# Performance work log

Measured on AMD Instinct MI355X. Metric: run time of the kernel, lower is better.

Reference implementation:

```python
import jax, jax.numpy as jnp
import numpy as np

B, HH, WW, C = 1, 96, 96, 128
HEADS, K = 4, 7

def setup_inputs() -> dict:
    key = jax.random.key(0)
    ks = jax.random.split(key, 6)
    def lin(k, o, i):
        return jax.random.normal(k, (o, i), jnp.float32) * (1.0 / np.sqrt(i))
    return {
        "x": jax.random.normal(ks[0], (B, HH, WW, C), jnp.float32),
        "qkv_w": lin(ks[1], 3 * C, C),
        "qkv_b": jnp.zeros((3 * C,), jnp.float32),
        "proj_w": lin(ks[2], C, C),
        "proj_b": jnp.zeros((C,), jnp.float32),
        "fc1_w": lin(ks[3], 4 * C, C),
        "fc1_b": jnp.zeros((4 * C,), jnp.float32),
        "fc2_w": lin(ks[4], C, 4 * C),
        "fc2_b": jnp.zeros((C,), jnp.float32),
    }

def _na2d(q, k, v):
    # q,k,v: [B, heads, H, W, hd]; NATTEN 2D neighborhood attention,
    # kernel K, stride 1, dilation 1, non-causal. Windows are clamped at
    # borders so each query attends to exactly K*K in-bounds keys.
    Bq, h, Hs, Ws, hd = q.shape
    start_h = jnp.clip(jnp.arange(Hs) - K // 2, 0, Hs - K)
    idx_h = start_h[:, None] + jnp.arange(K)  # [H, K]
    start_w = jnp.clip(jnp.arange(Ws) - K // 2, 0, Ws - K)
    idx_w = start_w[:, None] + jnp.arange(K)  # [W, K]
    I = idx_h[:, None, :, None]  # -> [H, W, K, K] broadcast
    J = idx_w[None, :, None, :]
    k_nb = k[:, :, I, J, :]  # [B, heads, H, W, K, K, hd]
    v_nb = v[:, :, I, J, :]
    scale = jnp.asarray(hd, q.dtype) ** -0.5
    logits = jnp.einsum('bhijd,bhijkld->bhijkl', q, k_nb) * scale
    attn = jax.nn.softmax(logits.reshape(Bq, h, Hs, Ws, K * K), axis=-1)
    attn = attn.reshape(Bq, h, Hs, Ws, K, K)
    return jnp.einsum('bhijkl,bhijkld->bhijd', attn, v_nb)

def reference(x, qkv_w, qkv_b, proj_w, proj_b, fc1_w, fc1_b, fc2_w, fc2_b):
    Bq, Hs, Ws, Cc = x.shape
    hd = Cc // HEADS
    qkv = x @ qkv_w.T + qkv_b  # [B,H,W,3C]
    q, k, v = jnp.split(qkv, 3, axis=-1)
    def to_heads(t):
        return t.reshape(Bq, Hs, Ws, HEADS, hd).transpose(0, 3, 1, 2, 4)
    o = _na2d(to_heads(q), to_heads(k), to_heads(v))  # [B,heads,H,W,hd]
    o = o.transpose(0, 2, 3, 1, 4).reshape(Bq, Hs, Ws, Cc)
    x0 = o @ proj_w.T + proj_b
    h1 = jax.nn.gelu(x0 @ fc1_w.T + fc1_b, approximate=False)
    return h1 @ fc2_w.T + fc2_b
```

## Files before the change

kernel.cpp:

```cpp
#include <hip/hip_runtime.h>

typedef __bf16 bf16_t;
typedef __bf16 bf16x8 __attribute__((ext_vector_type(8)));
typedef __bf16 bf16x4 __attribute__((ext_vector_type(4)));
typedef float f32x4 __attribute__((ext_vector_type(4)));

#define HH 96
#define WW 96
#define CC 128
#define HEADS 4
#define HD 32
#define TOK (HH * WW)
#define PLANE (TOK * CC)
#define KW 7
#define KK 49

#define W_QKV 0
#define W_PROJ 49152
#define W_FC1 65536
#define W_FC2 131072
#define W_TOT 196608

__device__ __forceinline__ bf16x8 cvt8(const float* __restrict__ p) {
    const f32x4 a = *(const f32x4*)p;
    const f32x4 b = *(const f32x4*)(p + 4);
    bf16x8 r;
    r[0] = (bf16_t)a[0]; r[1] = (bf16_t)a[1]; r[2] = (bf16_t)a[2]; r[3] = (bf16_t)a[3];
    r[4] = (bf16_t)b[0]; r[5] = (bf16_t)b[1]; r[6] = (bf16_t)b[2]; r[7] = (bf16_t)b[3];
    return r;
}

template <int NT>
__device__ __forceinline__ void mmaN(const bf16_t* __restrict__ A, int lda,
                                     const bf16_t* __restrict__ W, int ldb,
                                     int K, f32x4* acc) {
    const int lane = threadIdx.x & 63;
    const bf16_t* ap = A + (lane & 15) * lda + ((lane >> 4) * 8);
    const bf16_t* bp = W + (lane & 15) * ldb + ((lane >> 4) * 8);
    for (int k0 = 0; k0 < K; k0 += 32) {
        bf16x8 a = *(const bf16x8*)(ap + k0);
#pragma unroll
        for (int t = 0; t < NT; t++) {
            bf16x8 b = *(const bf16x8*)(bp + t * 16 * ldb + k0);
            acc[t] = __builtin_amdgcn_mfma_f32_16x16x32_bf16(a, b, acc[t], 0, 0, 0);
        }
    }
}

__global__ __launch_bounds__(256) void k_cvt(const float* __restrict__ qkv_w,
                                             const float* __restrict__ proj_w,
                                             const float* __restrict__ fc1_w,
                                             const float* __restrict__ fc2_w,
                                             bf16_t* __restrict__ wb) {
    const int base = (blockIdx.x * 256 + threadIdx.x) * 4;
    const float* src;
    if (base < W_PROJ)      src = qkv_w + base;
    else if (base < W_FC1)  src = proj_w + (base - W_PROJ);
    else if (base < W_FC2)  src = fc1_w + (base - W_FC1);
    else                    src = fc2_w + (base - W_FC2);
    const f32x4 a = *(const f32x4*)src;
    bf16x4 r;
    r[0] = (bf16_t)a[0]; r[1] = (bf16_t)a[1]; r[2] = (bf16_t)a[2]; r[3] = (bf16_t)a[3];
    *(bf16x4*)(wb + base) = r;
}

__global__ __launch_bounds__(256) void k_qkv(const float* __restrict__ x,
                                             const bf16_t* __restrict__ wb,
                                             const float* __restrict__ bias,
                                             bf16_t* __restrict__ q,
                                             bf16_t* __restrict__ k,
                                             bf16_t* __restrict__ v) {
    const int wid = blockIdx.x * 4 + (threadIdx.x >> 6);
    const int m0 = (wid / 6) * 16;
    const int n0 = (wid % 6) * 64;
    const int lane = threadIdx.x & 63;
    const float* ap = x + (m0 + (lane & 15)) * CC + ((lane >> 4) * 8);
    const bf16_t* bp = wb + (n0 + (lane & 15)) * CC + ((lane >> 4) * 8);
    f32x4 acc[4] = {};
    for (int k0 = 0; k0 < CC; k0 += 32) {
        bf16x8 a = cvt8(ap + k0);
#pragma unroll
        for (int t = 0; t < 4; t++) {
            bf16x8 b = *(const bf16x8*)(bp + t * 16 * CC + k0);
            acc[t] = __builtin_amdgcn_mfma_f32_16x16x32_bf16(a, b, acc[t], 0, 0, 0);
        }
    }
#pragma unroll
    for (int t = 0; t < 4; t++) {
        const int n = n0 + t * 16 + (lane & 15);
        const float bb = bias[n];
        const int part = n >> 7;
        const int c = n & 127;
        bf16_t* dst = (part == 0) ? q : (part == 1) ? k : v;
#pragma unroll
        for (int r = 0; r < 4; r++) {
            const int m = m0 + (lane >> 4) * 4 + r;
            dst[m * CC + c] = (bf16_t)(acc[t][r] + bb);
        }
    }
}

#define PATCH 10
#define PSZ 100
#define NPAD 112
#define STR 136
__global__ __launch_bounds__(256) void k_na2d(bf16_t* __restrict__ qo,
                                              const bf16_t* __restrict__ kg,
                                              const bf16_t* __restrict__ vg) {
    __shared__ __align__(16) bf16_t regA[(NPAD + 16) * STR];
    __shared__ __align__(16) bf16_t Pbuf[4 * 16 * STR];
    bf16_t* ks  = regA;
    bf16_t* qs  = regA + NPAD * STR;
    bf16_t* vst = regA;

    const int tid = threadIdx.x;
    const int w = tid >> 6, lane = tid & 63;
    const int g = lane >> 4, li = lane & 15;
    const int bi = blockIdx.x / 24, bj = blockIdx.x % 24;
    const int i0 = bi * 4, j0 = bj * 4;
    const int pr0 = min(max(i0 - 3, 0), HH - PATCH);
    const int pc0 = min(max(j0 - 3, 0), WW - PATCH);

    for (int idx = tid; idx < PSZ * 16; idx += 256) {
        const int row = idx >> 4, c8 = idx & 15;
        const int pi = row / PATCH, pj = row - PATCH * pi;
        *(bf16x8*)(ks + row * STR + c8 * 8) =
            *(const bf16x8*)(kg + ((pr0 + pi) * WW + (pc0 + pj)) * CC + c8 * 8);
    }
    {
        const int row = tid >> 4, c8 = tid & 15;
        const int ti = row >> 2, tj = row & 3;
        *(bf16x8*)(qs + row * STR + c8 * 8) =
            *(const bf16x8*)(qo + ((i0 + ti) * WW + (j0 + tj)) * CC + c8 * 8);
    }
    __syncthreads();

    const int head = w;
    f32x4 lg[7];
    {
        const bf16x8 aq = *(const bf16x8*)(qs + li * STR + head * HD + g * 8);
#pragma unroll
        for (int t = 0; t < 7; t++) {
            const bf16x8 bk = *(const bf16x8*)(ks + (t * 16 + li) * STR + head * HD + g * 8);
            lg[t] = __builtin_amdgcn_mfma_f32_16x16x32_bf16(aq, bk, (f32x4){0.f,0.f,0.f,0.f}, 0, 0, 0);
        }
    }

    int lr[4], lc[4];
#pragma unroll
    for (int r = 0; r < 4; r++) {
        const int m = g * 4 + r;
        const int i = i0 + (m >> 2), j = j0 + (m & 3);
        lr[r] = min(max(i - 3, 0), HH - KW) - pr0;
        lc[r] = min(max(j - 3, 0), WW - KW) - pc0;
    }
    const float scale = 0.17677669529663687f;
#pragma unroll
    for (int t = 0; t < 7; t++) {
        const int col = t * 16 + li;
        const int pi = col / PATCH, pj = col - PATCH * pi;
#pragma unroll
        for (int r = 0; r < 4; r++) {
            const bool valid = (col < PSZ) &&
                               ((unsigned)(pi - lr[r]) <= 6u) &&
                               ((unsigned)(pj - lc[r]) <= 6u);
            lg[t][r] = valid ? lg[t][r] * scale : -1e30f;
        }
    }
    f32x4 mx = lg[0], sm;
#pragma unroll
    for (int t = 1; t < 7; t++)
#pragma unroll
        for (int r = 0; r < 4; r++) mx[r] = fmaxf(mx[r], lg[t][r]);
#pragma unroll
    for (int off = 8; off; off >>= 1)
#pragma unroll
        for (int r = 0; r < 4; r++) mx[r] = fmaxf(mx[r], __shfl_xor(mx[r], off));
#pragma unroll
    for (int r = 0; r < 4; r++) sm[r] = 0.f;
#pragma unroll
    for (int t = 0; t < 7; t++)
#pragma unroll
        for (int r = 0; r < 4; r++) {
            lg[t][r] = __expf(lg[t][r] - mx[r]);
            sm[r] += lg[t][r];
        }
#pragma unroll
    for (int off = 8; off; off >>= 1)
#pragma unroll
        for (int r = 0; r < 4; r++) sm[r] += __shfl_xor(sm[r], off);
#pragma unroll
    for (int r = 0; r < 4; r++) sm[r] = 1.f / sm[r];

    bf16_t* Pw = Pbuf + w * 16 * STR;
#pragma unroll
    for (int t = 0; t < 7; t++)
#pragma unroll
        for (int r = 0; r < 4; r++)
            Pw[(g * 4 + r) * STR + t * 16 + li] = (bf16_t)(lg[t][r] * sm[r]);
    *(bf16x4*)(Pw + (lane >> 2) * STR + NPAD + (lane & 3) * 4) = (bf16x4){0,0,0,0};

    __syncthreads();
    for (int idx = tid; idx < PSZ * 16; idx += 256) {
        const int c8 = idx / PSZ;
        const int p  = idx - c8 * PSZ;
        const int pi = p / PATCH, pj = p - PATCH * pi;
        const bf16x8 t = *(const bf16x8*)(vg + ((pr0 + pi) * WW + (pc0 + pj)) * CC + c8 * 8);
#pragma unroll
        for (int e = 0; e < 8; e++) vst[(c8 * 8 + e) * STR + p] = t[e];
    }
    for (int idx = tid; idx < 128 * 8; idx += 256) {
        const int row = idx >> 3, c4 = idx & 7;
        *(bf16x4*)(vst + row * STR + PSZ + c4 * 4) = (bf16x4){0,0,0,0};
    }
    __syncthreads();

    f32x4 oA[2] = {};
#pragma unroll
    for (int ks0 = 0; ks0 < 128; ks0 += 32) {
        const bf16x8 a = *(const bf16x8*)(Pw + li * STR + ks0 + g * 8);
#pragma unroll
        for (int t2 = 0; t2 < 2; t2++) {
            const bf16x8 b = *(const bf16x8*)(vst + (head * HD + t2 * 16 + li) * STR + ks0 + g * 8);
            oA[t2] = __builtin_amdgcn_mfma_f32_16x16x32_bf16(a, b, oA[t2], 0, 0, 0);
        }
    }
#pragma unroll
    for (int t2 = 0; t2 < 2; t2++)
#pragma unroll
        for (int r = 0; r < 4; r++) {
            const int m = g * 4 + r;
            const int i = i0 + (m >> 2), j = j0 + (m & 3);
            qo[(i * WW + j) * CC + head * HD + t2 * 16 + li] = (bf16_t)oA[t2][r];
        }
}

__global__ __launch_bounds__(256) void k_proj(const bf16_t* __restrict__ o,
                                              const bf16_t* __restrict__ wb,
                                              const float* __restrict__ bias,
                                              bf16_t* __restrict__ x0) {
    const int wid = blockIdx.x * 4 + (threadIdx.x >> 6);
    const int m0 = (wid / 2) * 16;
    const int n0 = (wid % 2) * 64;
    f32x4 acc[4] = {};
    mmaN<4>(o + m0 * CC, CC, wb + n0 * CC, CC, CC, acc);
    const int lane = threadIdx.x & 63;
#pragma unroll
    for (int t = 0; t < 4; t++) {
        const int n = n0 + t * 16 + (lane & 15);
        const float bb = bias[n];
#pragma unroll
        for (int r = 0; r < 4; r++) {
            const int m = m0 + (lane >> 4) * 4 + r;
            x0[m * CC + n] = (bf16_t)(acc[t][r] + bb);
        }
    }
}

#define H1S 520
__global__ __launch_bounds__(256) void k_mlp(const bf16_t* __restrict__ x0,
                                             const bf16_t* __restrict__ w1,
                                             const float* __restrict__ b1,
                                             const bf16_t* __restrict__ w2,
                                             const float* __restrict__ b2,
                                             float* __restrict__ out) {
    __shared__ __align__(16) bf16_t h1s[16 * H1S];
    const int wv = threadIdx.x >> 6;
    const int lane = threadIdx.x & 63;
    const int m0 = blockIdx.x * 16;

    {
        f32x4 acc[8] = {};
        mmaN<8>(x0 + m0 * CC, CC, w1 + (wv * 128) * CC, CC, CC, acc);
#pragma unroll
        for (int t = 0; t < 8; t++) {
            const int n = wv * 128 + t * 16 + (lane & 15);
            const float bb = b1[n];
#pragma unroll
            for (int r = 0; r < 4; r++) {
                const int m = (lane >> 4) * 4 + r;
                const float xv = acc[t][r] + bb;
                const float u = 0.7978845608028654f * (xv + 0.044715f * xv * xv * xv);
                const float e = __expf(2.f * u);
                const float gg = 0.5f * xv * (2.f - 2.f / (e + 1.f));
                h1s[m * H1S + n] = (bf16_t)gg;
            }
        }
    }
    __syncthreads();

    {
        f32x4 acc[2] = {};
        mmaN<2>(h1s, H1S, w2 + (wv * 32) * (4 * CC), 4 * CC, 4 * CC, acc);
#pragma unroll
        for (int t = 0; t < 2; t++) {
            const int n = wv * 32 + t * 16 + (lane & 15);
            const float bb = b2[n];
#pragma unroll
            for (int r = 0; r < 4; r++) {
                const int m = (lane >> 4) * 4 + r;
                float xv = acc[t][r] + bb;
                xv = fminf(fmaxf(xv, -1e4f), 1e4f);
                out[(m0 + m) * CC + n] = xv;
            }
        }
    }
}

extern "C" void kernel_launch(void* const* d_in, const int* in_sizes, int n_in,
                              void* d_out, int out_size, void* d_ws, size_t ws_size,
                              hipStream_t stream) {
    const float* x      = (const float*)d_in[0];
    const float* qkv_w  = (const float*)d_in[1];
    const float* qkv_b  = (const float*)d_in[2];
    const float* proj_w = (const float*)d_in[3];
    const float* proj_b = (const float*)d_in[4];
    const float* fc1_w  = (const float*)d_in[5];
    const float* fc1_b  = (const float*)d_in[6];
    const float* fc2_w  = (const float*)d_in[7];
    const float* fc2_b  = (const float*)d_in[8];

    bf16_t* qo = (bf16_t*)d_out;
    bf16_t* ws = (bf16_t*)d_ws;
    bf16_t* kb = ws;
    bf16_t* vb = ws + PLANE;
    bf16_t* wb = ws + 2 * PLANE;
    bf16_t* x0 = kb;

    k_cvt <<<192,  256, 0, stream>>>(qkv_w, proj_w, fc1_w, fc2_w, wb);
    k_qkv <<<864,  256, 0, stream>>>(x, wb + W_QKV, qkv_b, qo, kb, vb);
    k_na2d<<<576,  256, 0, stream>>>(qo, kb, vb);
    k_proj<<<288,  256, 0, stream>>>(qo, wb + W_PROJ, proj_b, x0);
    k_mlp <<<576,  256, 0, stream>>>(x0, wb + W_FC1, fc1_b, wb + W_FC2, fc2_b,
                                     (float*)d_out);
}
```

Baseline: 130.9 us.

## Fuse neighborhood attention, projection and MLP into one kernel; fold weight conversion into QKV

Collapses five launches into two. The weight-conversion kernel is merged into the QKV GEMM, which now converts qkv_w from fp32 on the fly and writes Q as fp32 into the output buffer. The attention kernel then runs the output projection, fc1+GELU and fc2 on its 16-token tile in shared memory, so the o and x0 intermediates never go through global memory. In exchange each attention block does more serial work with more syncs, and QKV blocks re-convert fp32 qkv weights per block.

```diff
diff --git a/kernel.cpp b/kernel.cpp
--- a/kernel.cpp
+++ b/kernel.cpp
@@ -13,13 +13,21 @@
 #define TOK (HH * WW)
 #define PLANE (TOK * CC)
 #define KW 7
-#define KK 49
-
-#define W_QKV 0
-#define W_PROJ 49152
-#define W_FC1 65536
-#define W_FC2 131072
-#define W_TOT 196608
+
+#define W_PROJ 0
+#define W_FC1  16384
+#define W_FC2  81920
+#define W_TOT  147456
+
+#define PATCH 10
+#define PSZ 100
+#define NPAD 112
+#define STR 136
+#define H1S 520
+
+#define REGA_ELE ((NPAD + 16) * STR)
+#define PBUF_ELE (4 * 16 * STR)
+#define SMEM_BYTES ((REGA_ELE + PBUF_ELE) * 2)
 
 __device__ __forceinline__ bf16x8 cvt8(const float* __restrict__ p) {
     const f32x4 a = *(const f32x4*)p;
@@ -47,79 +55,88 @@
     }
 }
 
-__global__ __launch_bounds__(256) void k_cvt(const float* __restrict__ qkv_w,
+__global__ __launch_bounds__(256) void k_qkv(const float* __restrict__ x,
+                                             const float* __restrict__ qkv_w,
+                                             const float* __restrict__ qkv_b,
                                              const float* __restrict__ proj_w,
                                              const float* __restrict__ fc1_w,
                                              const float* __restrict__ fc2_w,
+                                             float* __restrict__ qf,
+                                             bf16_t* __restrict__ kb,
+                                             bf16_t* __restrict__ vb,
                                              bf16_t* __restrict__ wb) {
-    const int base = (blockIdx.x * 256 + threadIdx.x) * 4;
-    const float* src;
-    if (base < W_PROJ)      src = qkv_w + base;
-    else if (base < W_FC1)  src = proj_w + (base - W_PROJ);
-    else if (base < W_FC2)  src = fc1_w + (base - W_FC1);
-    else                    src = fc2_w + (base - W_FC2);
-    const f32x4 a = *(const f32x4*)src;
-    bf16x4 r;
-    r[0] = (bf16_t)a[0]; r[1] = (bf16_t)a[1]; r[2] = (bf16_t)a[2]; r[3] = (bf16_t)a[3];
-    *(bf16x4*)(wb + base) = r;
-}
-
-__global__ __launch_bounds__(256) void k_qkv(const float* __restrict__ x,
-                                             const bf16_t* __restrict__ wb,
-                                             const float* __restrict__ bias,
-                                             bf16_t* __restrict__ q,
-                                             bf16_t* __restrict__ k,
-                                             bf16_t* __restrict__ v) {
-    const int wid = blockIdx.x * 4 + (threadIdx.x >> 6);
-    const int m0 = (wid / 6) * 16;
-    const int n0 = (wid % 6) * 64;
-    const int lane = threadIdx.x & 63;
-    const float* ap = x + (m0 + (lane & 15)) * CC + ((lane >> 4) * 8);
-    const bf16_t* bp = wb + (n0 + (lane & 15)) * CC + ((lane >> 4) * 8);
-    f32x4 acc[4] = {};
+    const int tid = threadIdx.x, bid = blockIdx.x;
+    {
+        const int idx = bid * 256 + tid;
+        if (idx < W_TOT / 4) {
+            const int base = idx * 4;
+            const float* src;
+            if (base < W_FC1)      src = proj_w + base;
+            else if (base < W_FC2) src = fc1_w + (base - W_FC1);
+            else                   src = fc2_w + (base - W_FC2);
+            const f32x4 a = *(const f32x4*)src;
+            bf16x4 r;
+            r[0] = (bf16_t)a[0]; r[1] = (bf16_t)a[1];
+            r[2] = (bf16_t)a[2]; r[3] = (bf16_t)a[3];
+            *(bf16x4*)(wb + base) = r;
+        }
+    }
+    const int w = tid >> 6, lane = tid & 63;
+    const int g = lane >> 4, li = lane & 15;
+    const int m0 = bid * 16;
+    const float* ap = x + (m0 + li) * CC + g * 8;
+    const float* bp = qkv_w + (w * 96 + li) * CC + g * 8;
+    f32x4 acc[6] = {};
     for (int k0 = 0; k0 < CC; k0 += 32) {
         bf16x8 a = cvt8(ap + k0);
 #pragma unroll
-        for (int t = 0; t < 4; t++) {
-            bf16x8 b = *(const bf16x8*)(bp + t * 16 * CC + k0);
+        for (int t = 0; t < 6; t++) {
+            bf16x8 b = cvt8(bp + t * 16 * CC + k0);
             acc[t] = __builtin_amdgcn_mfma_f32_16x16x32_bf16(a, b, acc[t], 0, 0, 0);
         }
     }
 #pragma unroll
-    for (int t = 0; t < 4; t++) {
-        const int n = n0 + t * 16 + (lane & 15);
-        const float bb = bias[n];
-        const int part = n >> 7;
-        const int c = n & 127;
-        bf16_t* dst = (part == 0) ? q : (part == 1) ? k : v;
+    for (int t = 0; t < 6; t++) {
+        const int n = w * 96 + t * 16 + li;
+        const float bb = qkv_b[n];
+        const int part = n >> 7, c = n & 127;
 #pragma unroll
         for (int r = 0; r < 4; r++) {
-            const int m = m0 + (lane >> 4) * 4 + r;
-            dst[m * CC + c] = (bf16_t)(acc[t][r] + bb);
-        }
-    }
-}
-
-#define PATCH 10
-#define PSZ 100
-#define NPAD 112
-#define STR 136
-__global__ __launch_bounds__(256) void k_na2d(bf16_t* __restrict__ qo,
-                                              const bf16_t* __restrict__ kg,
-                                              const bf16_t* __restrict__ vg) {
-    __shared__ __align__(16) bf16_t regA[(NPAD + 16) * STR];
-    __shared__ __align__(16) bf16_t Pbuf[4 * 16 * STR];
-    bf16_t* ks  = regA;
-    bf16_t* qs  = regA + NPAD * STR;
-    bf16_t* vst = regA;
+            const int m = m0 + g * 4 + r;
+            const float val = acc[t][r] + bb;
+            if (part == 0)      qf[m * CC + c] = val;
+            else if (part == 1) kb[m * CC + c] = (bf16_t)val;
+            else                vb[m * CC + c] = (bf16_t)val;
+        }
+    }
+}
+
+__global__ __launch_bounds__(256, 3) void k_attn_mlp(
+        float* __restrict__ qof,
+        const bf16_t* __restrict__ kg,
+        const bf16_t* __restrict__ vg,
+        const bf16_t* __restrict__ wb,
+        const float* __restrict__ proj_b,
+        const float* __restrict__ fc1_b,
+        const float* __restrict__ fc2_b) {
+    __shared__ __align__(16) bf16_t smem[REGA_ELE + PBUF_ELE];
+    bf16_t* ks   = smem;
+    bf16_t* qs   = smem + NPAD * STR;
+    bf16_t* vst  = smem;
+    bf16_t* h1s  = smem;
+    bf16_t* Pbuf = smem + REGA_ELE;
+    bf16_t* o_s  = Pbuf;
+    bf16_t* x0s  = Pbuf + 16 * STR;
 
     const int tid = threadIdx.x;
     const int w = tid >> 6, lane = tid & 63;
     const int g = lane >> 4, li = lane & 15;
-    const int bi = blockIdx.x / 24, bj = blockIdx.x % 24;
+    const int bid = blockIdx.x;
+    const int bi = bid / 24, bj = bid % 24;
     const int i0 = bi * 4, j0 = bj * 4;
     const int pr0 = min(max(i0 - 3, 0), HH - PATCH);
     const int pc0 = min(max(j0 - 3, 0), WW - PATCH);
+    const int head = w;
 
     for (int idx = tid; idx < PSZ * 16; idx += 256) {
         const int row = idx >> 4, c8 = idx & 15;
@@ -131,11 +148,10 @@
         const int row = tid >> 4, c8 = tid & 15;
         const int ti = row >> 2, tj = row & 3;
         *(bf16x8*)(qs + row * STR + c8 * 8) =
-            *(const bf16x8*)(qo + ((i0 + ti) * WW + (j0 + tj)) * CC + c8 * 8);
-    }
-    __syncthreads();
-
-    const int head = w;
+            cvt8(qof + ((i0 + ti) * WW + (j0 + tj)) * CC + c8 * 8);
+    }
+    __syncthreads();
+
     f32x4 lg[7];
     {
         const bf16x8 aq = *(const bf16x8*)(qs + li * STR + head * HD + g * 8);
@@ -145,7 +161,6 @@
             lg[t] = __builtin_amdgcn_mfma_f32_16x16x32_bf16(aq, bk, (f32x4){0.f,0.f,0.f,0.f}, 0, 0, 0);
         }
     }
-
     int lr[4], lc[4];
 #pragma unroll
     for (int r = 0; r < 4; r++) {
@@ -199,11 +214,10 @@
         for (int r = 0; r < 4; r++)
             Pw[(g * 4 + r) * STR + t * 16 + li] = (bf16_t)(lg[t][r] * sm[r]);
     *(bf16x4*)(Pw + (lane >> 2) * STR + NPAD + (lane & 3) * 4) = (bf16x4){0,0,0,0};
-
-    __syncthreads();
+    __syncthreads();
+
     for (int idx = tid; idx < PSZ * 16; idx += 256) {
-        const int c8 = idx / PSZ;
-        const int p  = idx - c8 * PSZ;
+        const int c8 = idx / PSZ, p = idx - c8 * PSZ;
         const int pi = p / PATCH, pj = p - PATCH * pi;
         const bf16x8 t = *(const bf16x8*)(vg + ((pr0 + pi) * WW + (pc0 + pj)) * CC + c8 * 8);
 #pragma unroll
@@ -225,60 +239,39 @@
             oA[t2] = __builtin_amdgcn_mfma_f32_16x16x32_bf16(a, b, oA[t2], 0, 0, 0);
         }
     }
+    __syncthreads();
+
 #pragma unroll
     for (int t2 = 0; t2 < 2; t2++)
 #pragma unroll
-        for (int r = 0; r < 4; r++) {
-            const int m = g * 4 + r;
-            const int i = i0 + (m >> 2), j = j0 + (m & 3);
-            qo[(i * WW + j) * CC + head * HD + t2 * 16 + li] = (bf16_t)oA[t2][r];
-        }
-}
-
-__global__ __launch_bounds__(256) void k_proj(const bf16_t* __restrict__ o,
-                                              const bf16_t* __restrict__ wb,
-                                              const float* __restrict__ bias,
-                                              bf16_t* __restrict__ x0) {
-    const int wid = blockIdx.x * 4 + (threadIdx.x >> 6);
-    const int m0 = (wid / 2) * 16;
-    const int n0 = (wid % 2) * 64;
-    f32x4 acc[4] = {};
-    mmaN<4>(o + m0 * CC, CC, wb + n0 * CC, CC, CC, acc);
-    const int lane = threadIdx.x & 63;
-#pragma unroll
-    for (int t = 0; t < 4; t++) {
-        const int n = n0 + t * 16 + (lane & 15);
-        const float bb = bias[n];
-#pragma unroll
-        for (int r = 0; r < 4; r++) {
-            const int m = m0 + (lane >> 4) * 4 + r;
-            x0[m * CC + n] = (bf16_t)(acc[t][r] + bb);
-        }
-    }
-}
-
-#define H1S 520
-__global__ __launch_bounds__(256) void k_mlp(const bf16_t* __restrict__ x0,
-                                             const bf16_t* __restrict__ w1,
-                                             const float* __restrict__ b1,
-                                             const bf16_t* __restrict__ w2,
-                                             const float* __restrict__ b2,
-                                             float* __restrict__ out) {
-    __shared__ __align__(16) bf16_t h1s[16 * H1S];
-    const int wv = threadIdx.x >> 6;
-    const int lane = threadIdx.x & 63;
-    const int m0 = blockIdx.x * 16;
+        for (int r = 0; r < 4; r++)
+            o_s[(g * 4 + r) * STR + head * HD + t2 * 16 + li] = (bf16_t)oA[t2][r];
+    __syncthreads();
+
+    {
+        f32x4 acc[2] = {};
+        mmaN<2>(o_s, STR, wb + W_PROJ + (w * 32) * CC, CC, CC, acc);
+#pragma unroll
+        for (int t = 0; t < 2; t++) {
+            const int n = w * 32 + t * 16 + li;
+            const float bb = proj_b[n];
+#pragma unroll
+            for (int r = 0; r < 4; r++)
+                x0s[(g * 4 + r) * STR + n] = (bf16_t)(acc[t][r] + bb);
+        }
+    }
+    __syncthreads();
 
     {
         f32x4 acc[8] = {};
-        mmaN<8>(x0 + m0 * CC, CC, w1 + (wv * 128) * CC, CC, CC, acc);
+        mmaN<8>(x0s, STR, wb + W_FC1 + (w * 128) * CC, CC, CC, acc);
 #pragma unroll
         for (int t = 0; t < 8; t++) {
-            const int n = wv * 128 + t * 16 + (lane & 15);
-            const float bb = b1[n];
+            const int n = w * 128 + t * 16 + li;
+            const float bb = fc1_b[n];
 #pragma unroll
             for (int r = 0; r < 4; r++) {
-                const int m = (lane >> 4) * 4 + r;
+                const int m = g * 4 + r;
                 const float xv = acc[t][r] + bb;
                 const float u = 0.7978845608028654f * (xv + 0.044715f * xv * xv * xv);
                 const float e = __expf(2.f * u);
@@ -291,17 +284,18 @@
 
     {
         f32x4 acc[2] = {};
-        mmaN<2>(h1s, H1S, w2 + (wv * 32) * (4 * CC), 4 * CC, 4 * CC, acc);
+        mmaN<2>(h1s, H1S, wb + W_FC2 + (w * 32) * (4 * CC), 4 * CC, 4 * CC, acc);
 #pragma unroll
         for (int t = 0; t < 2; t++) {
-            const int n = wv * 32 + t * 16 + (lane & 15);
-            const float bb = b2[n];
+            const int n = w * 32 + t * 16 + li;
+            const float bb = fc2_b[n];
 #pragma unroll
             for (int r = 0; r < 4; r++) {
-                const int m = (lane >> 4) * 4 + r;
+                const int m = g * 4 + r;
+                const int i = i0 + (m >> 2), j = j0 + (m & 3);
                 float xv = acc[t][r] + bb;
                 xv = fminf(fmaxf(xv, -1e4f), 1e4f);
-                out[(m0 + m) * CC + n] = xv;
+                qof[(i * WW + j) * CC + n] = xv;
             }
         }
     }
@@ -320,17 +314,13 @@
     const float* fc2_w  = (const float*)d_in[7];
     const float* fc2_b  = (const float*)d_in[8];
 
-    bf16_t* qo = (bf16_t*)d_out;
+    float* qof = (float*)d_out;
     bf16_t* ws = (bf16_t*)d_ws;
     bf16_t* kb = ws;
     bf16_t* vb = ws + PLANE;
     bf16_t* wb = ws + 2 * PLANE;
-    bf16_t* x0 = kb;
-
-    k_cvt <<<192,  256, 0, stream>>>(qkv_w, proj_w, fc1_w, fc2_w, wb);
-    k_qkv <<<864,  256, 0, stream>>>(x, wb + W_QKV, qkv_b, qo, kb, vb);
-    k_na2d<<<576,  256, 0, stream>>>(qo, kb, vb);
-    k_proj<<<288,  256, 0, stream>>>(qo, wb + W_PROJ, proj_b, x0);
-    k_mlp <<<576,  256, 0, stream>>>(x0, wb + W_FC1, fc1_b, wb + W_FC2, fc2_b,
-                                     (float*)d_out);
-}
+
+    k_qkv     <<<576, 256, 0, stream>>>(x, qkv_w, qkv_b, proj_w, fc1_w, fc2_w,
+                                        qof, kb, vb, wb);
+    k_attn_mlp<<<576, 256, 0, stream>>>(qof, kb, vb, wb, proj_b, fc1_b, fc2_b);
+}
```

Measured after the change: 129.3 us. No clear change (-1.2%).
